# Kernel optimization log

Hardware: AMD Instinct MI355X
Metric: run time of the kernel (lower is better)

Reference implementation:

```python
import jax, jax.numpy as jnp
import numpy as np

STAGE_NUM = 3
BN_EPS = 1e-5

def _l2norm(t, axis):
    return t / (1e-6 + jnp.linalg.norm(t, axis=axis, keepdims=True))

def setup_inputs() -> dict:
    key = jax.random.key(0)
    ks = jax.random.split(key, 5)
    b, c, h, w, k = 16, 512, 64, 64, 64
    x = jax.random.normal(ks[0], (b, c, h, w), jnp.float32)
    mu = jax.random.normal(ks[1], (1, c, k), jnp.float32) * np.sqrt(2.0 / k)
    mu = _l2norm(mu, axis=1)
    conv1_w = jax.random.normal(ks[2], (c, c), jnp.float32) * np.sqrt(2.0 / c)
    conv1_b = jnp.zeros((c,), jnp.float32)
    conv2_w = jax.random.normal(ks[3], (c, c), jnp.float32) * np.sqrt(2.0 / c)
    bn_gamma = jnp.ones((c,), jnp.float32)
    bn_beta = jnp.zeros((c,), jnp.float32)
    return {"x": x, "mu": mu, "conv1_w": conv1_w, "conv1_b": conv1_b,
            "conv2_w": conv2_w, "bn_gamma": bn_gamma, "bn_beta": bn_beta}

def reference(x, mu, conv1_w, conv1_b, conv2_w, bn_gamma, bn_beta):
    b, c, h, w = x.shape
    idn = x
    # conv1: 1x1 conv == per-pixel matmul
    xf = jnp.einsum('oc,bchw->bohw', conv1_w, x) + conv1_b[None, :, None, None]
    xf = xf.reshape(b, c, h * w)            # [b,c,n]
    mu_b = jnp.broadcast_to(mu, (b, c, mu.shape[2]))  # [b,c,k]
    z = None
    for _ in range(STAGE_NUM):
        z = jax.nn.softmax(jnp.einsum('bcn,bck->bnk', xf, mu_b), axis=2)  # [b,n,k]
        z_ = z / (1e-6 + jnp.sum(z, axis=1, keepdims=True))
        mu_b = _l2norm(jnp.einsum('bcn,bnk->bck', xf, z_), axis=1)
    # torch.no_grad(): mu and z are constants w.r.t. autodiff
    mu_b = jax.lax.stop_gradient(mu_b)
    z = jax.lax.stop_gradient(z)
    recon = jnp.einsum('bck,bnk->bcn', mu_b, z).reshape(b, c, h, w)
    recon = jax.nn.relu(recon)
    # conv2 (1x1, no bias) + BatchNorm2d (training: batch stats, biased var)
    y = jnp.einsum('oc,bchw->bohw', conv2_w, recon)
    mean = jnp.mean(y, axis=(0, 2, 3), keepdims=True)
    var = jnp.var(y, axis=(0, 2, 3), keepdims=True)
    y = (y - mean) * jax.lax.rsqrt(var + BN_EPS)
    y = y * bn_gamma[None, :, None, None] + bn_beta[None, :, None, None]
    return jax.nn.relu(y + idn)
```

## Files before the change

### kernel.cpp

```cpp
#include <hip/hip_runtime.h>
#include <math.h>

#define CDIM 512
#define NDIM 4096
#define KDIM 64
#define BDIM 16
#define NSPLIT 8

typedef __attribute__((ext_vector_type(8))) _Float16 f16x8;
typedef __attribute__((ext_vector_type(4))) _Float16 f16x4;
typedef __attribute__((ext_vector_type(4))) float f32x4;

__device__ __forceinline__ void g2lds16(const void* g, void* l) {
  __builtin_amdgcn_global_load_lds(
      (const __attribute__((address_space(1))) int*)g,
      (__attribute__((address_space(3))) int*)l, 16, 0, 0);
}

__device__ __forceinline__ f16x8 ldsfrag(const short* base, int row, int kk,
                                         int lh) {
  int slot = (kk * 4 + lh) ^ (row & 7);
  return *reinterpret_cast<const f16x8*>(&base[row * 64 + slot * 8]);
}

__global__ __launch_bounds__(256) void k_cvtT16(const float* __restrict__ in,
                                                _Float16* __restrict__ outT) {
  __shared__ __align__(16) _Float16 T[64][80];
  const int t = threadIdx.x;
  const int n0 = blockIdx.x * 64, c0 = blockIdx.y * 64;
  const float* ib = in + (size_t)blockIdx.z * CDIM * NDIM;
  _Float16* ob = outT + (size_t)blockIdx.z * NDIM * CDIM;
#pragma unroll
  for (int i = 0; i < 4; ++i) {
    int idx = i * 256 + t;
    int cl = idx >> 4, f4 = idx & 15;
    float4 v = *reinterpret_cast<const float4*>(
        &ib[(size_t)(c0 + cl) * NDIM + n0 + f4 * 4]);
    T[f4 * 4 + 0][cl] = (_Float16)v.x;
    T[f4 * 4 + 1][cl] = (_Float16)v.y;
    T[f4 * 4 + 2][cl] = (_Float16)v.z;
    T[f4 * 4 + 3][cl] = (_Float16)v.w;
  }
  __syncthreads();
#pragma unroll
  for (int i = 0; i < 2; ++i) {
    int idx = i * 256 + t;
    int nl = idx >> 3, ch = idx & 7;
    uint4 u = *reinterpret_cast<const uint4*>(&T[nl][ch * 8]);
    *reinterpret_cast<uint4*>(&ob[(size_t)(n0 + nl) * CDIM + c0 + ch * 8]) = u;
  }
}

__global__ void k_cvt_w16(const float* __restrict__ w,
                          _Float16* __restrict__ wh) {
  int i = (blockIdx.x * 256 + threadIdx.x) * 4;
  float4 v = *reinterpret_cast<const float4*>(&w[i]);
  wh[i] = (_Float16)v.x; wh[i + 1] = (_Float16)v.y;
  wh[i + 2] = (_Float16)v.z; wh[i + 3] = (_Float16)v.w;
}

__global__ __launch_bounds__(256) void k_conv1_16(
    const _Float16* __restrict__ xT, const _Float16* __restrict__ w1,
    const float* __restrict__ b1, _Float16* __restrict__ xfT,
    _Float16* __restrict__ xf) {
  __shared__ __align__(16) short smem[17408];
  short* At = smem;
  short* Bt = smem + 8192;
  const int tid = threadIdx.x;
  const int l = tid & 63, w = tid >> 6;
  const int wm = w >> 1, wn = w & 1;
  const int lr = l & 15, lh = l >> 4;
  const int i0 = blockIdx.x * 128;
  const int j0 = blockIdx.y * 128;
  const int b = blockIdx.z;
  const short* Ag = (const short*)(xT + (size_t)b * NDIM * CDIM);
  const short* Bg = (const short*)w1;
  f32x4 acc[4][4] = {};
  for (int c0 = 0; c0 < CDIM; c0 += 64) {
#pragma unroll
    for (int i = 0; i < 4; ++i) {
      int slot = i * 256 + tid;
      int r = slot >> 3, s = slot & 7, sp = s ^ (r & 7);
      g2lds16(Ag + (size_t)(i0 + r) * CDIM + c0 + sp * 8, At + slot * 8);
    }
#pragma unroll
    for (int i = 0; i < 4; ++i) {
      int slot = i * 256 + tid;
      int r = slot >> 3, s = slot & 7, sp = s ^ (r & 7);
      g2lds16(Bg + (size_t)(j0 + r) * CDIM + c0 + sp * 8, Bt + slot * 8);
    }
    __syncthreads();
#pragma unroll
    for (int kk = 0; kk < 2; ++kk) {
      f16x8 af[4], bf[4];
#pragma unroll
      for (int m = 0; m < 4; ++m) af[m] = ldsfrag(At, wm * 64 + m * 16 + lr, kk, lh);
#pragma unroll
      for (int nf = 0; nf < 4; ++nf) bf[nf] = ldsfrag(Bt, wn * 64 + nf * 16 + lr, kk, lh);
#pragma unroll
      for (int m = 0; m < 4; ++m)
#pragma unroll
        for (int nf = 0; nf < 4; ++nf)
          acc[m][nf] = __builtin_amdgcn_mfma_f32_16x16x32_f16(af[m], bf[nf],
                                                              acc[m][nf], 0, 0, 0);
    }
    __syncthreads();
  }
  _Float16* Otf = (_Float16*)smem;
  _Float16* ob = xfT + (size_t)b * NDIM * CDIM;
#pragma unroll
  for (int m = 0; m < 4; ++m) {
#pragma unroll
    for (int nf = 0; nf < 4; ++nf) {
      int ol = wn * 64 + nf * 16 + lr;
      float bv = b1[j0 + ol];
#pragma unroll
      for (int r = 0; r < 4; ++r) {
        int nl = wm * 64 + m * 16 + lh * 4 + r;
        _Float16 hv = (_Float16)(acc[m][nf][r] + bv);
        ob[(size_t)(i0 + nl) * CDIM + j0 + ol] = hv;
        Otf[ol * 136 + nl] = hv;
      }
    }
  }
  __syncthreads();
  _Float16* xfb = xf + (size_t)b * CDIM * NDIM;
#pragma unroll
  for (int i = 0; i < 8; ++i) {
    int seg = i * 256 + tid;
    int row = seg >> 4, cs = seg & 15;
    f16x8 v = *reinterpret_cast<const f16x8*>(&Otf[row * 136 + cs * 8]);
    *reinterpret_cast<f16x8*>(&xfb[(size_t)(j0 + row) * NDIM + i0 + cs * 8]) = v;
  }
}

__global__ __launch_bounds__(256) void k_conv2_16(
    const _Float16* __restrict__ w2, const _Float16* __restrict__ reconT,
    _Float16* __restrict__ y16, float* __restrict__ bnsum,
    float* __restrict__ bnsumsq) {
  __shared__ __align__(16) short At[128 * 64];
  __shared__ __align__(16) short Bt[128 * 64];
  __shared__ float bns[128], bnq[128];
  const int tid = threadIdx.x;
  const int l = tid & 63, w = tid >> 6;
  const int wm = w >> 1, wn = w & 1;
  const int lr = l & 15, lh = l >> 4;
  const int i0 = blockIdx.y * 128;
  const int j0 = blockIdx.x * 128;
  const int b = blockIdx.z;
  if (tid < 128) { bns[tid] = 0.f; bnq[tid] = 0.f; }
  const short* Ag = (const short*)w2;
  const short* Bg = (const short*)(reconT + (size_t)b * NDIM * CDIM);
  f32x4 acc[4][4] = {};
  for (int c0 = 0; c0 < CDIM; c0 += 64) {
#pragma unroll
    for (int i = 0; i < 4; ++i) {
      int slot = i * 256 + tid;
      int r = slot >> 3, s = slot & 7, sp = s ^ (r & 7);
      g2lds16(Ag + (size_t)(i0 + r) * CDIM + c0 + sp * 8, At + slot * 8);
    }
#pragma unroll
    for (int i = 0; i < 4; ++i) {
      int slot = i * 256 + tid;
      int r = slot >> 3, s = slot & 7, sp = s ^ (r & 7);
      g2lds16(Bg + (size_t)(j0 + r) * CDIM + c0 + sp * 8, Bt + slot * 8);
    }
    __syncthreads();
#pragma unroll
    for (int kk = 0; kk < 2; ++kk) {
      f16x8 af[4], bf[4];
#pragma unroll
      for (int m = 0; m < 4; ++m) af[m] = ldsfrag(At, wm * 64 + m * 16 + lr, kk, lh);
#pragma unroll
      for (int nf = 0; nf < 4; ++nf) bf[nf] = ldsfrag(Bt, wn * 64 + nf * 16 + lr, kk, lh);
#pragma unroll
      for (int m = 0; m < 4; ++m)
#pragma unroll
        for (int nf = 0; nf < 4; ++nf)
          acc[m][nf] = __builtin_amdgcn_mfma_f32_16x16x32_f16(af[m], bf[nf],
                                                              acc[m][nf], 0, 0, 0);
    }
    __syncthreads();
  }
  _Float16* yb = y16 + (size_t)b * CDIM * NDIM;
#pragma unroll
  for (int m = 0; m < 4; ++m) {
#pragma unroll
    for (int r = 0; r < 4; ++r) {
      int ol = wm * 64 + m * 16 + lh * 4 + r;
      float ps = 0.f, pq = 0.f;
#pragma unroll
      for (int nf = 0; nf < 4; ++nf) {
        float v = acc[m][nf][r];
        ps += v; pq += v * v;
        yb[(size_t)(i0 + ol) * NDIM + j0 + wn * 64 + nf * 16 + lr] = (_Float16)v;
      }
#pragma unroll
      for (int d = 1; d < 16; d <<= 1) {
        ps += __shfl_xor(ps, d);
        pq += __shfl_xor(pq, d);
      }
      if (lr == 0) { atomicAdd(&bns[ol], ps); atomicAdd(&bnq[ol], pq); }
    }
  }
  __syncthreads();
  if (tid < 128) {
    atomicAdd(&bnsum[i0 + tid], bns[tid]);
    atomicAdd(&bnsumsq[i0 + tid], bnq[tid]);
  }
}

__global__ void k_init_mu16(const float* __restrict__ mu,
                            _Float16* __restrict__ muT) {
  int idx = blockIdx.x * 256 + threadIdx.x;
  int rem = idx & 32767;
  int k = rem >> 9, c = rem & 511;
  muT[idx] = (_Float16)mu[c * KDIM + k];
}

__global__ __launch_bounds__(256) void k_s1_16(const _Float16* __restrict__ xfT,
                                               const _Float16* __restrict__ muT,
                                               _Float16* __restrict__ z,
                                               _Float16* __restrict__ zT,
                                               float* __restrict__ colsum) {
  __shared__ __align__(16) short At[128 * 64];
  __shared__ __align__(16) short Bt[64 * 64];
  __shared__ __align__(16) _Float16 zs[128][72];
  __shared__ float csum[4][64];
  const int tid = threadIdx.x;
  const int l = tid & 63, w = tid >> 6;
  const int lr = l & 15, lh = l >> 4;
  const int n0 = blockIdx.x * 128;
  const int b = blockIdx.y;
  const short* Ag = (const short*)(xfT + (size_t)b * NDIM * CDIM);
  const short* Bg = (const short*)(muT + (size_t)b * KDIM * CDIM);
  f32x4 acc[2][4] = {};
  for (int c0 = 0; c0 < CDIM; c0 += 64) {
#pragma unroll
    for (int i = 0; i < 4; ++i) {
      int slot = i * 256 + tid;
      int r = slot >> 3, s = slot & 7, sp = s ^ (r & 7);
      g2lds16(Ag + (size_t)(n0 + r) * CDIM + c0 + sp * 8, At + slot * 8);
    }
#pragma unroll
    for (int i = 0; i < 2; ++i) {
      int slot = i * 256 + tid;
      int r = slot >> 3, s = slot & 7, sp = s ^ (r & 7);
      g2lds16(Bg + (size_t)r * CDIM + c0 + sp * 8, Bt + slot * 8);
    }
    __syncthreads();
#pragma unroll
    for (int kk = 0; kk < 2; ++kk) {
      f16x8 af[2], bf;
#pragma unroll
      for (int nf = 0; nf < 2; ++nf)
        af[nf] = ldsfrag(At, w * 32 + nf * 16 + lr, kk, lh);
#pragma unroll
      for (int kf = 0; kf < 4; ++kf) {
        bf = ldsfrag(Bt, kf * 16 + lr, kk, lh);
#pragma unroll
        for (int nf = 0; nf < 2; ++nf)
          acc[nf][kf] = __builtin_amdgcn_mfma_f32_16x16x32_f16(af[nf], bf,
                                                               acc[nf][kf], 0, 0, 0);
      }
    }
    __syncthreads();
  }
#pragma unroll
  for (int nf = 0; nf < 2; ++nf) {
#pragma unroll
    for (int r = 0; r < 4; ++r) {
      float m = fmaxf(fmaxf(acc[nf][0][r], acc[nf][1][r]),
                      fmaxf(acc[nf][2][r], acc[nf][3][r]));
#pragma unroll
      for (int d = 8; d >= 1; d >>= 1) m = fmaxf(m, __shfl_xor(m, d));
      float e[4], s = 0.f;
#pragma unroll
      for (int kf = 0; kf < 4; ++kf) { e[kf] = __expf(acc[nf][kf][r] - m); s += e[kf]; }
#pragma unroll
      for (int d = 8; d >= 1; d >>= 1) s += __shfl_xor(s, d);
      float inv = 1.f / s;
      int row = w * 32 + nf * 16 + lh * 4 + r;
#pragma unroll
      for (int kf = 0; kf < 4; ++kf)
        zs[row][kf * 16 + lr] = (_Float16)(e[kf] * inv);
    }
  }
  __syncthreads();
  _Float16* zb = z + (size_t)b * NDIM * KDIM;
  _Float16* zTb = zT + (size_t)b * KDIM * NDIM;
#pragma unroll
  for (int i = 0; i < 4; ++i) {
    int idx = i * 256 + tid;
    int n = idx >> 3, ch = idx & 7;
    *reinterpret_cast<uint4*>(&zb[(size_t)(n0 + n) * KDIM + ch * 8]) =
        *reinterpret_cast<const uint4*>(&zs[n][ch * 8]);
  }
#pragma unroll
  for (int i = 0; i < 4; ++i) {
    int idx = i * 256 + tid;
    int k = idx >> 4, nch = idx & 15;
    f16x8 v;
#pragma unroll
    for (int j = 0; j < 8; ++j) v[j] = zs[nch * 8 + j][k];
    *reinterpret_cast<f16x8*>(&zTb[(size_t)k * NDIM + n0 + nch * 8]) = v;
  }
  {
    int k = tid & 63, q = tid >> 6;
    float s = 0.f;
#pragma unroll
    for (int n = 0; n < 32; ++n) s += (float)zs[q * 32 + n][k];
    csum[q][k] = s;
  }
  __syncthreads();
  if (tid < 64)
    atomicAdd(&colsum[b * KDIM + tid],
              csum[0][tid] + csum[1][tid] + csum[2][tid] + csum[3][tid]);
}

__global__ __launch_bounds__(256) void k_s2_16(const _Float16* __restrict__ zT,
                                               const _Float16* __restrict__ xf,
                                               float* __restrict__ mupart) {
  __shared__ __align__(16) short At[64 * 64];
  __shared__ __align__(16) short Bt[128 * 64];
  const int tid = threadIdx.x;
  const int l = tid & 63, w = tid >> 6;
  const int lr = l & 15, lh = l >> 4;
  const int c0 = blockIdx.x * 128;
  const int split = blockIdx.y;
  const int b = blockIdx.z;
  const short* Ag = (const short*)(zT + (size_t)b * KDIM * NDIM);
  const short* Bg = (const short*)(xf + (size_t)b * CDIM * NDIM);
  f32x4 acc[4][2] = {};
  for (int st = 0; st < 8; ++st) {
    const int nb = split * (NDIM / NSPLIT) + st * 64;
#pragma unroll
    for (int i = 0; i < 2; ++i) {
      int slot = i * 256 + tid;
      int r = slot >> 3, s = slot & 7, sp = s ^ (r & 7);
      g2lds16(Ag + (size_t)r * NDIM + nb + sp * 8, At + slot * 8);
    }
#pragma unroll
    for (int i = 0; i < 4; ++i) {
      int slot = i * 256 + tid;
      int r = slot >> 3, s = slot & 7, sp = s ^ (r & 7);
      g2lds16(Bg + (size_t)(c0 + r) * NDIM + nb + sp * 8, Bt + slot * 8);
    }
    __syncthreads();
#pragma unroll
    for (int kk = 0; kk < 2; ++kk) {
      f16x8 bf[2], af;
#pragma unroll
      for (int cf = 0; cf < 2; ++cf)
        bf[cf] = ldsfrag(Bt, w * 32 + cf * 16 + lr, kk, lh);
#pragma unroll
      for (int kf = 0; kf < 4; ++kf) {
        af = ldsfrag(At, kf * 16 + lr, kk, lh);
#pragma unroll
        for (int cf = 0; cf < 2; ++cf)
          acc[kf][cf] = __builtin_amdgcn_mfma_f32_16x16x32_f16(af, bf[cf],
                                                               acc[kf][cf], 0, 0, 0);
      }
    }
    __syncthreads();
  }
  float* mp = mupart + ((size_t)(split * BDIM + b) * KDIM) * CDIM;
#pragma unroll
  for (int kf = 0; kf < 4; ++kf) {
    int k = kf * 16 + lh * 4;
#pragma unroll
    for (int r = 0; r < 4; ++r)
#pragma unroll
      for (int cf = 0; cf < 2; ++cf)
        mp[(size_t)(k + r) * CDIM + c0 + w * 32 + cf * 16 + lr] = acc[kf][cf][r];
  }
}

__global__ __launch_bounds__(256) void k_s2red(const float* __restrict__ mupart,
                                               const float* __restrict__ colsum,
                                               _Float16* __restrict__ muT,
                                               _Float16* __restrict__ mu_ck) {
  __shared__ float red[4];
  const int tid = threadIdx.x;
  const int b = blockIdx.x >> 6, k = blockIdx.x & 63;
  float v0 = 0.f, v1 = 0.f;
#pragma unroll
  for (int s = 0; s < NSPLIT; ++s) {
    const float* mp = mupart + ((size_t)(s * BDIM + b) * KDIM + k) * CDIM;
    v0 += mp[tid];
    v1 += mp[tid + 256];
  }
  float ssq = v0 * v0 + v1 * v1;
#pragma unroll
  for (int d = 32; d >= 1; d >>= 1) ssq += __shfl_down(ssq, d);
  if ((tid & 63) == 0) red[tid >> 6] = ssq;
  __syncthreads();
  float tot = red[0] + red[1] + red[2] + red[3];
  float scs = 1.f / (1e-6f + colsum[b * KDIM + k]);
  float inv = scs / (1e-6f + scs * sqrtf(tot));
  _Float16 o0 = (_Float16)(v0 * inv), o1 = (_Float16)(v1 * inv);
  muT[((size_t)b * KDIM + k) * CDIM + tid] = o0;
  muT[((size_t)b * KDIM + k) * CDIM + tid + 256] = o1;
  mu_ck[((size_t)b * CDIM + tid) * KDIM + k] = o0;
  mu_ck[((size_t)b * CDIM + tid + 256) * KDIM + k] = o1;
}

__global__ __launch_bounds__(256) void k_recon16(const _Float16* __restrict__ z,
                                                 const _Float16* __restrict__ mu_ck,
                                                 _Float16* __restrict__ reconT) {
  __shared__ __align__(16) short Az[128 * 64];
  __shared__ __align__(16) short Bm[128 * 64];
  const int tid = threadIdx.x;
  const int l = tid & 63, w = tid >> 6;
  const int wm = w >> 1, wn = w & 1;
  const int lr = l & 15, lh = l >> 4;
  const int n0 = blockIdx.x * 128;
  const int c0 = blockIdx.y * 128;
  const int b = blockIdx.z;
  const short* Ag = (const short*)(z + (size_t)b * NDIM * KDIM);
  const short* Bg = (const short*)(mu_ck + (size_t)b * CDIM * KDIM);
#pragma unroll
  for (int i = 0; i < 4; ++i) {
    int slot = i * 256 + tid;
    int r = slot >> 3, s = slot & 7, sp = s ^ (r & 7);
    g2lds16(Ag + (size_t)(n0 + r) * KDIM + sp * 8, Az + slot * 8);
  }
#pragma unroll
  for (int i = 0; i < 4; ++i) {
    int slot = i * 256 + tid;
    int r = slot >> 3, s = slot & 7, sp = s ^ (r & 7);
    g2lds16(Bg + (size_t)(c0 + r) * KDIM + sp * 8, Bm + slot * 8);
  }
  __syncthreads();
  f32x4 acc[4][4] = {};
#pragma unroll
  for (int kk = 0; kk < 2; ++kk) {
    f16x8 af[4], bf[4];
#pragma unroll
    for (int m = 0; m < 4; ++m) af[m] = ldsfrag(Az, wm * 64 + m * 16 + lr, kk, lh);
#pragma unroll
    for (int nf = 0; nf < 4; ++nf) bf[nf] = ldsfrag(Bm, wn * 64 + nf * 16 + lr, kk, lh);
#pragma unroll
    for (int m = 0; m < 4; ++m)
#pragma unroll
      for (int nf = 0; nf < 4; ++nf)
        acc[m][nf] = __builtin_amdgcn_mfma_f32_16x16x32_f16(af[m], bf[nf],
                                                            acc[m][nf], 0, 0, 0);
  }
  _Float16* ob = reconT + (size_t)b * NDIM * CDIM;
#pragma unroll
  for (int m = 0; m < 4; ++m) {
#pragma unroll
    for (int r = 0; r < 4; ++r) {
      int n = n0 + wm * 64 + m * 16 + lh * 4 + r;
#pragma unroll
      for (int nf = 0; nf < 4; ++nf) {
        int c = c0 + wn * 64 + nf * 16 + lr;
        ob[(size_t)n * CDIM + c] = (_Float16)fmaxf(acc[m][nf][r], 0.f);
      }
    }
  }
}

__global__ void k_final(float* __restrict__ out, const _Float16* __restrict__ y16,
                        const float* __restrict__ x,
                        const float* __restrict__ bnsum,
                        const float* __restrict__ bnsumsq,
                        const float* __restrict__ gamma,
                        const float* __restrict__ beta) {
  const float invM = 1.f / (BDIM * (float)NDIM);
  const size_t total4 = (size_t)BDIM * CDIM * NDIM / 4;
  for (size_t i4 = (size_t)blockIdx.x * 256 + threadIdx.x; i4 < total4;
       i4 += (size_t)gridDim.x * 256) {
    int c = (int)((i4 >> 10) & (CDIM - 1));
    float mean = bnsum[c] * invM;
    float var = bnsumsq[c] * invM - mean * mean;
    float sc = rsqrtf(var + 1e-5f) * gamma[c];
    float sh = beta[c] - mean * sc;
    f16x4 yv = *reinterpret_cast<const f16x4*>(&y16[i4 * 4]);
    float4 xv = reinterpret_cast<const float4*>(x)[i4];
    float4 o;
    o.x = fmaxf(fmaf((float)yv[0], sc, sh) + xv.x, 0.f);
    o.y = fmaxf(fmaf((float)yv[1], sc, sh) + xv.y, 0.f);
    o.z = fmaxf(fmaf((float)yv[2], sc, sh) + xv.z, 0.f);
    o.w = fmaxf(fmaf((float)yv[3], sc, sh) + xv.w, 0.f);
    reinterpret_cast<float4*>(out)[i4] = o;
  }
}

extern "C" void kernel_launch(void* const* d_in, const int* in_sizes, int n_in,
                              void* d_out, int out_size, void* d_ws,
                              size_t ws_size, hipStream_t stream) {
  const float* x = (const float*)d_in[0];
  const float* mu = (const float*)d_in[1];
  const float* w1 = (const float*)d_in[2];
  const float* b1 = (const float*)d_in[3];
  const float* w2 = (const float*)d_in[4];
  const float* gamma = (const float*)d_in[5];
  const float* beta = (const float*)d_in[6];
  float* out = (float*)d_out;

  _Float16* xfT = (_Float16*)d_out;
  _Float16* xf = (_Float16*)d_out + 33554432;

  _Float16* wsH = (_Float16*)d_ws;
  _Float16* xT = wsH;
  _Float16* reconT = wsH;
  _Float16* z = wsH + 33554432;
  _Float16* zT = z + 4194304;
  _Float16* muT = zT + 4194304;
  _Float16* mu_ck = muT + 524288;
  _Float16* w1h = mu_ck + 524288;
  _Float16* w2h = w1h + 262144;
  float* wsF = (float*)(w2h + 262144);
  float* mupart = wsF;
  float* colsum = mupart + 4194304;
  float* bnsum = colsum + 1024;
  float* bnsumsq = bnsum + 512;
  _Float16* y16 = (_Float16*)(bnsumsq + 512);

  k_cvtT16<<<dim3(NDIM / 64, CDIM / 64, BDIM), 256, 0, stream>>>(x, xT);
  k_cvt_w16<<<CDIM * CDIM / 1024, 256, 0, stream>>>(w1, w1h);
  k_cvt_w16<<<CDIM * CDIM / 1024, 256, 0, stream>>>(w2, w2h);

  k_conv1_16<<<dim3(NDIM / 128, CDIM / 128, BDIM), 256, 0, stream>>>(
      xT, w1h, b1, xfT, xf);
  k_init_mu16<<<2048, 256, 0, stream>>>(mu, muT);

  for (int s = 0; s < 3; ++s) {
    hipMemsetAsync(colsum, 0, 1024 * sizeof(float), stream);
    k_s1_16<<<dim3(NDIM / 128, BDIM), 256, 0, stream>>>(xfT, muT, z, zT, colsum);
    k_s2_16<<<dim3(CDIM / 128, NSPLIT, BDIM), 256, 0, stream>>>(zT, xf, mupart);
    k_s2red<<<KDIM * BDIM, 256, 0, stream>>>(mupart, colsum, muT, mu_ck);
  }

  k_recon16<<<dim3(NDIM / 128, CDIM / 128, BDIM), 256, 0, stream>>>(z, mu_ck,
                                                                    reconT);
  hipMemsetAsync(bnsum, 0, 1024 * sizeof(float), stream);
  k_conv2_16<<<dim3(NDIM / 128, CDIM / 128, BDIM), 256, 0, stream>>>(
      w2h, reconT, y16, bnsum, bnsumsq);

  k_final<<<4096, 256, 0, stream>>>(out, y16, x, bnsum, bnsumsq, gamma, beta);
}
```

Baseline: 382.4 us.

## Fuse recon and conv2 into one kernel and atomically accumulate mu partials

Fuses the reconstruction GEMM (z·mu, relu) with the conv2 GEMM so the relu'd reconstruction tile stays in LDS instead of round-tripping through a large global buffer. The fused block holds a 128x512 fp16 tile in LDS and reads w2 fragments straight from global memory. Separately, the mu-update split partials are now atomically added into one buffer (zeroed per stage), removing the NSPLIT reduction in k_s2red. Risks are low occupancy from the large LDS footprint, uncached global weight loads, and atomic contention.

```diff
diff --git a/kernel.cpp b/kernel.cpp
--- a/kernel.cpp
+++ b/kernel.cpp
@@ -134,82 +134,6 @@
   }
 }
 
-__global__ __launch_bounds__(256) void k_conv2_16(
-    const _Float16* __restrict__ w2, const _Float16* __restrict__ reconT,
-    _Float16* __restrict__ y16, float* __restrict__ bnsum,
-    float* __restrict__ bnsumsq) {
-  __shared__ __align__(16) short At[128 * 64];
-  __shared__ __align__(16) short Bt[128 * 64];
-  __shared__ float bns[128], bnq[128];
-  const int tid = threadIdx.x;
-  const int l = tid & 63, w = tid >> 6;
-  const int wm = w >> 1, wn = w & 1;
-  const int lr = l & 15, lh = l >> 4;
-  const int i0 = blockIdx.y * 128;
-  const int j0 = blockIdx.x * 128;
-  const int b = blockIdx.z;
-  if (tid < 128) { bns[tid] = 0.f; bnq[tid] = 0.f; }
-  const short* Ag = (const short*)w2;
-  const short* Bg = (const short*)(reconT + (size_t)b * NDIM * CDIM);
-  f32x4 acc[4][4] = {};
-  for (int c0 = 0; c0 < CDIM; c0 += 64) {
-#pragma unroll
-    for (int i = 0; i < 4; ++i) {
-      int slot = i * 256 + tid;
-      int r = slot >> 3, s = slot & 7, sp = s ^ (r & 7);
-      g2lds16(Ag + (size_t)(i0 + r) * CDIM + c0 + sp * 8, At + slot * 8);
-    }
-#pragma unroll
-    for (int i = 0; i < 4; ++i) {
-      int slot = i * 256 + tid;
-      int r = slot >> 3, s = slot & 7, sp = s ^ (r & 7);
-      g2lds16(Bg + (size_t)(j0 + r) * CDIM + c0 + sp * 8, Bt + slot * 8);
-    }
-    __syncthreads();
-#pragma unroll
-    for (int kk = 0; kk < 2; ++kk) {
-      f16x8 af[4], bf[4];
-#pragma unroll
-      for (int m = 0; m < 4; ++m) af[m] = ldsfrag(At, wm * 64 + m * 16 + lr, kk, lh);
-#pragma unroll
-      for (int nf = 0; nf < 4; ++nf) bf[nf] = ldsfrag(Bt, wn * 64 + nf * 16 + lr, kk, lh);
-#pragma unroll
-      for (int m = 0; m < 4; ++m)
-#pragma unroll
-        for (int nf = 0; nf < 4; ++nf)
-          acc[m][nf] = __builtin_amdgcn_mfma_f32_16x16x32_f16(af[m], bf[nf],
-                                                              acc[m][nf], 0, 0, 0);
-    }
-    __syncthreads();
-  }
-  _Float16* yb = y16 + (size_t)b * CDIM * NDIM;
-#pragma unroll
-  for (int m = 0; m < 4; ++m) {
-#pragma unroll
-    for (int r = 0; r < 4; ++r) {
-      int ol = wm * 64 + m * 16 + lh * 4 + r;
-      float ps = 0.f, pq = 0.f;
-#pragma unroll
-      for (int nf = 0; nf < 4; ++nf) {
-        float v = acc[m][nf][r];
-        ps += v; pq += v * v;
-        yb[(size_t)(i0 + ol) * NDIM + j0 + wn * 64 + nf * 16 + lr] = (_Float16)v;
-      }
-#pragma unroll
-      for (int d = 1; d < 16; d <<= 1) {
-        ps += __shfl_xor(ps, d);
-        pq += __shfl_xor(pq, d);
-      }
-      if (lr == 0) { atomicAdd(&bns[ol], ps); atomicAdd(&bnq[ol], pq); }
-    }
-  }
-  __syncthreads();
-  if (tid < 128) {
-    atomicAdd(&bnsum[i0 + tid], bns[tid]);
-    atomicAdd(&bnsumsq[i0 + tid], bnq[tid]);
-  }
-}
-
 __global__ void k_init_mu16(const float* __restrict__ mu,
                             _Float16* __restrict__ muT) {
   int idx = blockIdx.x * 256 + threadIdx.x;
@@ -364,7 +288,7 @@
     }
     __syncthreads();
   }
-  float* mp = mupart + ((size_t)(split * BDIM + b) * KDIM) * CDIM;
+  float* mp = mupart + (size_t)b * KDIM * CDIM;
 #pragma unroll
   for (int kf = 0; kf < 4; ++kf) {
     int k = kf * 16 + lh * 4;
@@ -372,7 +296,8 @@
     for (int r = 0; r < 4; ++r)
 #pragma unroll
       for (int cf = 0; cf < 2; ++cf)
-        mp[(size_t)(k + r) * CDIM + c0 + w * 32 + cf * 16 + lr] = acc[kf][cf][r];
+        atomicAdd(&mp[(size_t)(k + r) * CDIM + c0 + w * 32 + cf * 16 + lr],
+                  acc[kf][cf][r]);
   }
 }
 
@@ -383,13 +308,9 @@
   __shared__ float red[4];
   const int tid = threadIdx.x;
   const int b = blockIdx.x >> 6, k = blockIdx.x & 63;
-  float v0 = 0.f, v1 = 0.f;
-#pragma unroll
-  for (int s = 0; s < NSPLIT; ++s) {
-    const float* mp = mupart + ((size_t)(s * BDIM + b) * KDIM + k) * CDIM;
-    v0 += mp[tid];
-    v1 += mp[tid + 256];
-  }
+  const float* mp = mupart + ((size_t)b * KDIM + k) * CDIM;
+  float v0 = mp[tid];
+  float v1 = mp[tid + 256];
   float ssq = v0 * v0 + v1 * v1;
 #pragma unroll
   for (int d = 32; d >= 1; d >>= 1) ssq += __shfl_down(ssq, d);
@@ -405,58 +326,99 @@
   mu_ck[((size_t)b * CDIM + tid + 256) * KDIM + k] = o1;
 }
 
-__global__ __launch_bounds__(256) void k_recon16(const _Float16* __restrict__ z,
-                                                 const _Float16* __restrict__ mu_ck,
-                                                 _Float16* __restrict__ reconT) {
-  __shared__ __align__(16) short Az[128 * 64];
-  __shared__ __align__(16) short Bm[128 * 64];
+__global__ __launch_bounds__(512, 2) void k_rc2(
+    const _Float16* __restrict__ z, const _Float16* __restrict__ mu_ck,
+    const _Float16* __restrict__ w2, _Float16* __restrict__ y16,
+    float* __restrict__ bnsum, float* __restrict__ bnsumsq) {
+  __shared__ __align__(16) short R[128 * 512];
+  _Float16* Rh = (_Float16*)R;
   const int tid = threadIdx.x;
   const int l = tid & 63, w = tid >> 6;
-  const int wm = w >> 1, wn = w & 1;
-  const int lr = l & 15, lh = l >> 4;
+  const int lr = l & 15, lh = (l >> 4) & 3;
   const int n0 = blockIdx.x * 128;
-  const int c0 = blockIdx.y * 128;
-  const int b = blockIdx.z;
-  const short* Ag = (const short*)(z + (size_t)b * NDIM * KDIM);
-  const short* Bg = (const short*)(mu_ck + (size_t)b * CDIM * KDIM);
-#pragma unroll
-  for (int i = 0; i < 4; ++i) {
-    int slot = i * 256 + tid;
-    int r = slot >> 3, s = slot & 7, sp = s ^ (r & 7);
-    g2lds16(Ag + (size_t)(n0 + r) * KDIM + sp * 8, Az + slot * 8);
-  }
-#pragma unroll
-  for (int i = 0; i < 4; ++i) {
-    int slot = i * 256 + tid;
-    int r = slot >> 3, s = slot & 7, sp = s ^ (r & 7);
-    g2lds16(Bg + (size_t)(c0 + r) * KDIM + sp * 8, Bm + slot * 8);
+  const int b = blockIdx.y;
+
+  const short* zg = (const short*)(z + (size_t)b * NDIM * KDIM);
+  const short* mg = (const short*)(mu_ck + (size_t)b * CDIM * KDIM);
+  f16x8 zf[2];
+  {
+    const short* zrow = zg + (size_t)(n0 + w * 16 + lr) * KDIM;
+#pragma unroll
+    for (int kk = 0; kk < 2; ++kk)
+      zf[kk] = *reinterpret_cast<const f16x8*>(zrow + kk * 32 + lh * 8);
+  }
+#pragma unroll
+  for (int cc = 0; cc < 4; ++cc) {
+    f32x4 acc[8] = {};
+#pragma unroll
+    for (int kk = 0; kk < 2; ++kk) {
+#pragma unroll
+      for (int cf = 0; cf < 8; ++cf) {
+        const short* mrow = mg + (size_t)(cc * 128 + cf * 16 + lr) * KDIM;
+        f16x8 bf = *reinterpret_cast<const f16x8*>(mrow + kk * 32 + lh * 8);
+        acc[cf] = __builtin_amdgcn_mfma_f32_16x16x32_f16(zf[kk], bf, acc[cf],
+                                                         0, 0, 0);
+      }
+    }
+#pragma unroll
+    for (int cf = 0; cf < 8; ++cf) {
+#pragma unroll
+      for (int r = 0; r < 4; ++r) {
+        int n = w * 16 + lh * 4 + r;
+        int c = cc * 128 + cf * 16 + lr;
+        Rh[n * 512 + ((c >> 3) ^ (n & 7)) * 8 + (c & 7)] =
+            (_Float16)fmaxf(acc[cf][r], 0.f);
+      }
+    }
   }
   __syncthreads();
-  f32x4 acc[4][4] = {};
-#pragma unroll
-  for (int kk = 0; kk < 2; ++kk) {
-    f16x8 af[4], bf[4];
-#pragma unroll
-    for (int m = 0; m < 4; ++m) af[m] = ldsfrag(Az, wm * 64 + m * 16 + lr, kk, lh);
-#pragma unroll
-    for (int nf = 0; nf < 4; ++nf) bf[nf] = ldsfrag(Bm, wn * 64 + nf * 16 + lr, kk, lh);
-#pragma unroll
-    for (int m = 0; m < 4; ++m)
-#pragma unroll
-      for (int nf = 0; nf < 4; ++nf)
-        acc[m][nf] = __builtin_amdgcn_mfma_f32_16x16x32_f16(af[m], bf[nf],
-                                                            acc[m][nf], 0, 0, 0);
-  }
-  _Float16* ob = reconT + (size_t)b * NDIM * CDIM;
-#pragma unroll
-  for (int m = 0; m < 4; ++m) {
+
+  const short* wg = (const short*)w2;
+  _Float16* yb = y16 + (size_t)b * CDIM * NDIM;
+  f32x4 acc2[4][8] = {};
+  for (int cs = 0; cs < 8; ++cs) {
+#pragma unroll
+    for (int kk = 0; kk < 2; ++kk) {
+      f16x8 af[4], bf[8];
+#pragma unroll
+      for (int mf = 0; mf < 4; ++mf) {
+        const short* wrow = wg + (size_t)(w * 64 + mf * 16 + lr) * CDIM;
+        af[mf] = *reinterpret_cast<const f16x8*>(wrow + cs * 64 + kk * 32 + lh * 8);
+      }
+#pragma unroll
+      for (int nf = 0; nf < 8; ++nf) {
+        int n = nf * 16 + lr;
+        int slot = (cs * 8 + kk * 4 + lh) ^ (n & 7);
+        bf[nf] = *reinterpret_cast<const f16x8*>(&R[n * 512 + slot * 8]);
+      }
+#pragma unroll
+      for (int mf = 0; mf < 4; ++mf)
+#pragma unroll
+        for (int nf = 0; nf < 8; ++nf)
+          acc2[mf][nf] = __builtin_amdgcn_mfma_f32_16x16x32_f16(
+              af[mf], bf[nf], acc2[mf][nf], 0, 0, 0);
+    }
+  }
+#pragma unroll
+  for (int mf = 0; mf < 4; ++mf) {
 #pragma unroll
     for (int r = 0; r < 4; ++r) {
-      int n = n0 + wm * 64 + m * 16 + lh * 4 + r;
-#pragma unroll
-      for (int nf = 0; nf < 4; ++nf) {
-        int c = c0 + wn * 64 + nf * 16 + lr;
-        ob[(size_t)n * CDIM + c] = (_Float16)fmaxf(acc[m][nf][r], 0.f);
+      int o = w * 64 + mf * 16 + lh * 4 + r;
+      float ps = 0.f, pq = 0.f;
+#pragma unroll
+      for (int nf = 0; nf < 8; ++nf) {
+        float v = acc2[mf][nf][r];
+        ps += v; pq += v * v;
+        yb[(size_t)o * NDIM + n0 + nf * 16 + lr] = (_Float16)v;
+      }
+#pragma unroll
+      for (int d = 1; d < 16; d <<= 1) {
+        ps += __shfl_xor(ps, d);
+        pq += __shfl_xor(pq, d);
+      }
+      if (lr == 0) {
+        atomicAdd(&bnsum[o], ps);
+        atomicAdd(&bnsumsq[o], pq);
       }
     }
   }
@@ -505,7 +467,6 @@
 
   _Float16* wsH = (_Float16*)d_ws;
   _Float16* xT = wsH;
-  _Float16* reconT = wsH;
   _Float16* z = wsH + 33554432;
   _Float16* zT = z + 4194304;
   _Float16* muT = zT + 4194304;
@@ -514,7 +475,7 @@
   _Float16* w2h = w1h + 262144;
   float* wsF = (float*)(w2h + 262144);
   float* mupart = wsF;
-  float* colsum = mupart + 4194304;
+  float* colsum = mupart + 524288;
   float* bnsum = colsum + 1024;
   float* bnsumsq = bnsum + 512;
   _Float16* y16 = (_Float16*)(bnsumsq + 512);
@@ -530,15 +491,14 @@
   for (int s = 0; s < 3; ++s) {
     hipMemsetAsync(colsum, 0, 1024 * sizeof(float), stream);
     k_s1_16<<<dim3(NDIM / 128, BDIM), 256, 0, stream>>>(xfT, muT, z, zT, colsum);
+    hipMemsetAsync(mupart, 0, 524288 * sizeof(float), stream);
     k_s2_16<<<dim3(CDIM / 128, NSPLIT, BDIM), 256, 0, stream>>>(zT, xf, mupart);
     k_s2red<<<KDIM * BDIM, 256, 0, stream>>>(mupart, colsum, muT, mu_ck);
   }
 
-  k_recon16<<<dim3(NDIM / 128, CDIM / 128, BDIM), 256, 0, stream>>>(z, mu_ck,
-                                                                    reconT);
   hipMemsetAsync(bnsum, 0, 1024 * sizeof(float), stream);
-  k_conv2_16<<<dim3(NDIM / 128, CDIM / 128, BDIM), 256, 0, stream>>>(
-      w2h, reconT, y16, bnsum, bnsumsq);
+  k_rc2<<<dim3(NDIM / 128, BDIM), 512, 0, stream>>>(z, mu_ck, w2h, y16, bnsum,
+                                                    bnsumsq);
 
   k_final<<<4096, 256, 0, stream>>>(out, y16, x, bnsum, bnsumsq, gamma, beta);
 }
```

After: 453.6 us (median of 2 runs). +18.6%, slower.

## Fuse input fp32-to-fp16 transpose into conv1 loads and skip unused z writes

Applied to the files above, without the earlier changes.

Removes the separate transpose/convert kernel and has conv1 read fp32 x directly, converting it to fp16 and writing the swizzled LDS tile itself. This avoids one full write and read of the fp16 transposed input. The cost is that conv1 now uses strided scalar fp32 global loads instead of async 16-byte global-to-LDS copies, and it reads fp32 x once per output-channel tile (4 times) instead of fp16. Separately, the row-major z output is only written on the final EM stage, since earlier stages never use it.

```diff
diff --git a/kernel.cpp b/kernel.cpp
--- a/kernel.cpp
+++ b/kernel.cpp
@@ -21,34 +21,6 @@
                                          int lh) {
   int slot = (kk * 4 + lh) ^ (row & 7);
   return *reinterpret_cast<const f16x8*>(&base[row * 64 + slot * 8]);
-}
-
-__global__ __launch_bounds__(256) void k_cvtT16(const float* __restrict__ in,
-                                                _Float16* __restrict__ outT) {
-  __shared__ __align__(16) _Float16 T[64][80];
-  const int t = threadIdx.x;
-  const int n0 = blockIdx.x * 64, c0 = blockIdx.y * 64;
-  const float* ib = in + (size_t)blockIdx.z * CDIM * NDIM;
-  _Float16* ob = outT + (size_t)blockIdx.z * NDIM * CDIM;
-#pragma unroll
-  for (int i = 0; i < 4; ++i) {
-    int idx = i * 256 + t;
-    int cl = idx >> 4, f4 = idx & 15;
-    float4 v = *reinterpret_cast<const float4*>(
-        &ib[(size_t)(c0 + cl) * NDIM + n0 + f4 * 4]);
-    T[f4 * 4 + 0][cl] = (_Float16)v.x;
-    T[f4 * 4 + 1][cl] = (_Float16)v.y;
-    T[f4 * 4 + 2][cl] = (_Float16)v.z;
-    T[f4 * 4 + 3][cl] = (_Float16)v.w;
-  }
-  __syncthreads();
-#pragma unroll
-  for (int i = 0; i < 2; ++i) {
-    int idx = i * 256 + t;
-    int nl = idx >> 3, ch = idx & 7;
-    uint4 u = *reinterpret_cast<const uint4*>(&T[nl][ch * 8]);
-    *reinterpret_cast<uint4*>(&ob[(size_t)(n0 + nl) * CDIM + c0 + ch * 8]) = u;
-  }
 }
 
 __global__ void k_cvt_w16(const float* __restrict__ w,
@@ -60,7 +32,7 @@
 }
 
 __global__ __launch_bounds__(256) void k_conv1_16(
-    const _Float16* __restrict__ xT, const _Float16* __restrict__ w1,
+    const float* __restrict__ x, const _Float16* __restrict__ w1,
     const float* __restrict__ b1, _Float16* __restrict__ xfT,
     _Float16* __restrict__ xf) {
   __shared__ __align__(16) short smem[17408];
@@ -73,15 +45,21 @@
   const int i0 = blockIdx.x * 128;
   const int j0 = blockIdx.y * 128;
   const int b = blockIdx.z;
-  const short* Ag = (const short*)(xT + (size_t)b * NDIM * CDIM);
+  const float* xg = x + (size_t)b * CDIM * NDIM;
   const short* Bg = (const short*)w1;
+  const int an = tid & 127;
+  const int acg = tid >> 7;
   f32x4 acc[4][4] = {};
   for (int c0 = 0; c0 < CDIM; c0 += 64) {
 #pragma unroll
-    for (int i = 0; i < 4; ++i) {
-      int slot = i * 256 + tid;
-      int r = slot >> 3, s = slot & 7, sp = s ^ (r & 7);
-      g2lds16(Ag + (size_t)(i0 + r) * CDIM + c0 + sp * 8, At + slot * 8);
+    for (int cb = 0; cb < 4; ++cb) {
+      int c = acg * 32 + cb * 8;
+      f16x8 h;
+#pragma unroll
+      for (int j = 0; j < 8; ++j)
+        h[j] = (_Float16)xg[(size_t)(c0 + c + j) * NDIM + i0 + an];
+      int sp = ((c >> 3) ^ (an & 7));
+      *reinterpret_cast<f16x8*>(&At[an * 64 + sp * 8]) = h;
     }
 #pragma unroll
     for (int i = 0; i < 4; ++i) {
@@ -222,7 +200,8 @@
                                                const _Float16* __restrict__ muT,
                                                _Float16* __restrict__ z,
                                                _Float16* __restrict__ zT,
-                                               float* __restrict__ colsum) {
+                                               float* __restrict__ colsum,
+                                               int writeZ) {
   __shared__ __align__(16) short At[128 * 64];
   __shared__ __align__(16) short Bt[64 * 64];
   __shared__ __align__(16) _Float16 zs[128][72];
@@ -287,14 +266,16 @@
     }
   }
   __syncthreads();
-  _Float16* zb = z + (size_t)b * NDIM * KDIM;
   _Float16* zTb = zT + (size_t)b * KDIM * NDIM;
-#pragma unroll
-  for (int i = 0; i < 4; ++i) {
-    int idx = i * 256 + tid;
-    int n = idx >> 3, ch = idx & 7;
-    *reinterpret_cast<uint4*>(&zb[(size_t)(n0 + n) * KDIM + ch * 8]) =
-        *reinterpret_cast<const uint4*>(&zs[n][ch * 8]);
+  if (writeZ) {
+    _Float16* zb = z + (size_t)b * NDIM * KDIM;
+#pragma unroll
+    for (int i = 0; i < 4; ++i) {
+      int idx = i * 256 + tid;
+      int n = idx >> 3, ch = idx & 7;
+      *reinterpret_cast<uint4*>(&zb[(size_t)(n0 + n) * KDIM + ch * 8]) =
+          *reinterpret_cast<const uint4*>(&zs[n][ch * 8]);
+    }
   }
 #pragma unroll
   for (int i = 0; i < 4; ++i) {
@@ -504,7 +485,6 @@
   _Float16* xf = (_Float16*)d_out + 33554432;
 
   _Float16* wsH = (_Float16*)d_ws;
-  _Float16* xT = wsH;
   _Float16* reconT = wsH;
   _Float16* z = wsH + 33554432;
   _Float16* zT = z + 4194304;
@@ -519,17 +499,17 @@
   float* bnsumsq = bnsum + 512;
   _Float16* y16 = (_Float16*)(bnsumsq + 512);
 
-  k_cvtT16<<<dim3(NDIM / 64, CDIM / 64, BDIM), 256, 0, stream>>>(x, xT);
   k_cvt_w16<<<CDIM * CDIM / 1024, 256, 0, stream>>>(w1, w1h);
   k_cvt_w16<<<CDIM * CDIM / 1024, 256, 0, stream>>>(w2, w2h);
 
   k_conv1_16<<<dim3(NDIM / 128, CDIM / 128, BDIM), 256, 0, stream>>>(
-      xT, w1h, b1, xfT, xf);
+      x, w1h, b1, xfT, xf);
   k_init_mu16<<<2048, 256, 0, stream>>>(mu, muT);
 
   for (int s = 0; s < 3; ++s) {
     hipMemsetAsync(colsum, 0, 1024 * sizeof(float), stream);
-    k_s1_16<<<dim3(NDIM / 128, BDIM), 256, 0, stream>>>(xfT, muT, z, zT, colsum);
+    k_s1_16<<<dim3(NDIM / 128, BDIM), 256, 0, stream>>>(xfT, muT, z, zT, colsum,
+                                                        s == 2 ? 1 : 0);
     k_s2_16<<<dim3(CDIM / 128, NSPLIT, BDIM), 256, 0, stream>>>(zT, xf, mupart);
     k_s2red<<<KDIM * BDIM, 256, 0, stream>>>(mupart, colsum, muT, mu_ck);
   }
```

Result: slower. 403.7 us (+5.6%).
